# Optimization experiments

Hardware: AMD Instinct MI355X
Metric: run time of the kernel (lower is better)

Reference implementation:

```python
import jax, jax.numpy as jnp
import numpy as np

H = 64  # rnn_hidden_size


def _rnn_seq(x, W_ih, W_hh, b_ih, b_hh):
    """One tanh RNN layer over [B,T,D] -> full output sequence [B,T,H]."""
    pre = jnp.einsum('btd,hd->bth', x, W_ih) + b_ih  # input projection hoisted out of the scan
    h0 = jnp.zeros((x.shape[0], W_hh.shape[0]), x.dtype)
    def step(h, p_t):
        h = jnp.tanh(p_t + h @ W_hh.T + b_hh)
        return h, h
    _, ys = jax.lax.scan(step, h0, jnp.swapaxes(pre, 0, 1))  # scan over time
    return jnp.swapaxes(ys, 0, 1)


def _rnn_last(x, W_ih, W_hh, b_ih, b_hh):
    """One tanh RNN layer, returning only the last hidden state [B,H]."""
    pre = jnp.einsum('btd,hd->bth', x, W_ih) + b_ih
    h0 = jnp.zeros((x.shape[0], W_hh.shape[0]), x.dtype)
    def step(h, p_t):
        return jnp.tanh(p_t + h @ W_hh.T + b_hh), None
    h, _ = jax.lax.scan(step, h0, jnp.swapaxes(pre, 0, 1))
    return h


def setup_inputs() -> dict:
    key = jax.random.key(0)
    ks = jax.random.split(key, 32)
    B, T, D = 128, 4096, 3
    kr = 1.0 / np.sqrt(H)          # PyTorch RNN init bound
    u = lambda kk, shape, b: jax.random.uniform(kk, shape, jnp.float32, -b, b)
    inp = {
        'x': jax.random.normal(ks[0], (B, T, D), jnp.float32),
        'y': jax.random.normal(ks[1], (B, T, D), jnp.float32),
        'z': jax.random.normal(ks[2], (5,), jnp.float32),
        # rnn_empty, layer 0 (in=3) and layer 1 (in=64)
        'e_Wih0': u(ks[3], (H, D), kr), 'e_Whh0': u(ks[4], (H, H), kr),
        'e_bih0': u(ks[5], (H,), kr),  'e_bhh0': u(ks[6], (H,), kr),
        'e_Wih1': u(ks[7], (H, H), kr), 'e_Whh1': u(ks[8], (H, H), kr),
        'e_bih1': u(ks[9], (H,), kr),  'e_bhh1': u(ks[10], (H,), kr),
        # rnn_occupied
        'o_Wih0': u(ks[11], (H, D), kr), 'o_Whh0': u(ks[12], (H, H), kr),
        'o_bih0': u(ks[13], (H,), kr),  'o_bhh0': u(ks[14], (H,), kr),
        'o_Wih1': u(ks[15], (H, H), kr), 'o_Whh1': u(ks[16], (H, H), kr),
        'o_bih1': u(ks[17], (H,), kr),  'o_bhh1': u(ks[18], (H,), kr),
        # heads: fce/fco (64->2), fc1 (9->64), fc2 (64->5)
        'fce_w': u(ks[19], (2, H), kr), 'fce_b': u(ks[20], (2,), kr),
        'fco_w': u(ks[21], (2, H), kr), 'fco_b': u(ks[22], (2,), kr),
        'fc1_w': u(ks[23], (64, 9), 1.0 / np.sqrt(9)), 'fc1_b': u(ks[24], (64,), 1.0 / np.sqrt(9)),
        'fc2_w': u(ks[25], (5, 64), kr), 'fc2_b': u(ks[26], (5,), kr),
    }
    return inp


def reference(x, y, z,
              e_Wih0, e_Whh0, e_bih0, e_bhh0, e_Wih1, e_Whh1, e_bih1, e_bhh1,
              o_Wih0, o_Whh0, o_bih0, o_bhh0, o_Wih1, o_Whh1, o_bih1, o_bhh1,
              fce_w, fce_b, fco_w, fco_b, fc1_w, fc1_b, fc2_w, fc2_b):
    # two 2-layer tanh RNNs; last-timestep output of layer 2 == final hidden of layer 2
    hx = _rnn_last(_rnn_seq(x, e_Wih0, e_Whh0, e_bih0, e_bhh0),
                   e_Wih1, e_Whh1, e_bih1, e_bhh1)            # [B,H]
    hy = _rnn_last(_rnn_seq(y, o_Wih0, o_Whh0, o_bih0, o_bhh0),
                   o_Wih1, o_Whh1, o_bih1, o_bhh1)            # [B,H]
    e = hx @ fce_w.T + fce_b                                  # [B,2]
    o = hy @ fco_w.T + fco_b                                  # [B,2]
    zz = jnp.concatenate([e[0], o[0], z])                     # [9]
    h = jax.nn.relu(zz @ fc1_w.T + fc1_b)                     # [64]
    return h @ fc2_w.T + fc2_b                                # [5]
```

## Files before the change

kernel.cpp:

```cpp
#include <hip/hip_runtime.h>

#define T 4096
#define EP 8
#define RING 32
#define NEP (T / EP + 2)

typedef float f32x2 __attribute__((ext_vector_type(2)));
typedef unsigned long long u64;

__device__ __forceinline__ float fast_tanh(float x) {
    float e = __expf(2.0f * x);
    float r = __builtin_amdgcn_rcpf(e + 1.0f);
    return fmaf(-2.0f, r, 1.0f);
}

__device__ __forceinline__ float lane_bcast(float v, int j) {
    return __uint_as_float(__builtin_amdgcn_readlane(__float_as_uint(v), j));
}
__device__ __forceinline__ unsigned lane_bcast_u(float v, int j) {
    return (unsigned)__builtin_amdgcn_readlane(__float_as_uint(v), j);
}

#define PKFMA(acc, w, h) \
    asm("v_pk_fma_f32 %0, %1, %2, %0" : "+v"(acc) : "v"(w), "s"(h))

#define ANCHORP32(a) asm volatile("" : \
    "+v"((a)[0]),  "+v"((a)[1]),  "+v"((a)[2]),  "+v"((a)[3]),  \
    "+v"((a)[4]),  "+v"((a)[5]),  "+v"((a)[6]),  "+v"((a)[7]),  \
    "+v"((a)[8]),  "+v"((a)[9]),  "+v"((a)[10]), "+v"((a)[11]), \
    "+v"((a)[12]), "+v"((a)[13]), "+v"((a)[14]), "+v"((a)[15]), \
    "+v"((a)[16]), "+v"((a)[17]), "+v"((a)[18]), "+v"((a)[19]), \
    "+v"((a)[20]), "+v"((a)[21]), "+v"((a)[22]), "+v"((a)[23]), \
    "+v"((a)[24]), "+v"((a)[25]), "+v"((a)[26]), "+v"((a)[27]), \
    "+v"((a)[28]), "+v"((a)[29]), "+v"((a)[30]), "+v"((a)[31]))

#define ANCHOR16(a, b) asm volatile("" : \
    "+v"((a)[(b)+0]),  "+v"((a)[(b)+1]),  "+v"((a)[(b)+2]),  "+v"((a)[(b)+3]),  \
    "+v"((a)[(b)+4]),  "+v"((a)[(b)+5]),  "+v"((a)[(b)+6]),  "+v"((a)[(b)+7]),  \
    "+v"((a)[(b)+8]),  "+v"((a)[(b)+9]),  "+v"((a)[(b)+10]), "+v"((a)[(b)+11]), \
    "+v"((a)[(b)+12]), "+v"((a)[(b)+13]), "+v"((a)[(b)+14]), "+v"((a)[(b)+15]))
#define ANCHOR64(a) do { ANCHOR16(a, 0); ANCHOR16(a, 16); \
                         ANCHOR16(a, 32); ANCHOR16(a, 48); } while (0)

__device__ __forceinline__ u64 hpair(float hp, int j) {
    unsigned lo = lane_bcast_u(hp, j);
    unsigned hi = lane_bcast_u(hp, j + 1);
    return (u64)lo | ((u64)hi << 32);
}

__global__ void prep_kernel(const float* __restrict__ x, const float* __restrict__ y,
                            const float* __restrict__ eW, const float* __restrict__ ebi,
                            const float* __restrict__ ebh,
                            const float* __restrict__ oW, const float* __restrict__ obi,
                            const float* __restrict__ obh,
                            float* __restrict__ pre)
{
    int idx = blockIdx.x * blockDim.x + threadIdx.x;
    int i = idx & 63;
    int t = (idx >> 6) & (T - 1);
    int s = idx >> 18;
    const float* in = s ? y : x;
    const float* W  = s ? oW : eW;
    const float* bi = s ? obi : ebi;
    const float* bh = s ? obh : ebh;
    float v = bi[i] + bh[i]
            + W[i*3+0]*in[t*3+0] + W[i*3+1]*in[t*3+1] + W[i*3+2]*in[t*3+2];
    pre[idx] = v;
}

__global__ __launch_bounds__(256, 1) void seq_kernel(
    const float* __restrict__ pre,
    const float* __restrict__ eWhh0, const float* __restrict__ eWih1,
    const float* __restrict__ eWhh1, const float* __restrict__ ebih1,
    const float* __restrict__ ebhh1,
    const float* __restrict__ oWhh0, const float* __restrict__ oWih1,
    const float* __restrict__ oWhh1, const float* __restrict__ obih1,
    const float* __restrict__ obhh1,
    float* __restrict__ hlast)
{
    const int s    = blockIdx.x;
    const int wv   = threadIdx.x >> 6;
    const int lane = threadIdx.x & 63;

    __shared__ __align__(16) float h0ring[RING][64];
    __shared__ __align__(16) float qring[RING][64];

    const float* p = pre + s * T * 64;

    if (wv == 0) {
        const float* Whh0 = s ? oWhh0 : eWhh0;
        f32x2 w0p[32];
#pragma unroll
        for (int jp = 0; jp < 32; ++jp)
            w0p[jp] = ((const f32x2*)(Whh0 + lane * 64))[jp];

        float hp = 0.f;
        float pc[EP], pn[EP];
#pragma unroll
        for (int i = 0; i < EP; ++i) pc[i] = p[i * 64 + lane];

        for (int k = 0; k < NEP; ++k) {
            ANCHORP32(w0p);
            const int base = k * EP;
#pragma unroll
            for (int i = 0; i < EP; ++i) {
                int t = base + EP + i;
                pn[i] = (t < T) ? p[t * 64 + lane] : 0.f;
            }
            if (base < T) {
#pragma unroll
                for (int i = 0; i < EP; ++i) {
                    f32x2 acc0 = { pc[i], 0.f };
                    f32x2 acc1 = { 0.f, 0.f };
#pragma unroll
                    for (int jb = 0; jb < 64; jb += 8) {
                        u64 h01 = hpair(hp, jb + 0);
                        u64 h23 = hpair(hp, jb + 2);
                        u64 h45 = hpair(hp, jb + 4);
                        u64 h67 = hpair(hp, jb + 6);
                        PKFMA(acc0, w0p[(jb >> 1) + 0], h01);
                        PKFMA(acc1, w0p[(jb >> 1) + 1], h23);
                        PKFMA(acc0, w0p[(jb >> 1) + 2], h45);
                        PKFMA(acc1, w0p[(jb >> 1) + 3], h67);
                    }
                    hp = fast_tanh((acc0.x + acc0.y) + (acc1.x + acc1.y));
                    h0ring[(base + i) & (RING - 1)][lane] = hp;
                }
            }
#pragma unroll
            for (int i = 0; i < EP; ++i) pc[i] = pn[i];
            __syncthreads();
        }
    } else if (wv <= 2) {
        const float* Wih1 = s ? oWih1 : eWih1;
        const float  b1   = s ? (obih1[lane] + obhh1[lane])
                              : (ebih1[lane] + ebhh1[lane]);
        float wi[64];
#pragma unroll
        for (int j = 0; j < 64; ++j) wi[j] = Wih1[lane * 64 + j];

        const int i0 = (wv - 1) * (EP / 2);

        for (int k = 0; k < NEP; ++k) {
            ANCHOR64(wi);
            const int base = k * EP - EP;
            if (base >= 0 && base < T) {
#pragma unroll
                for (int i = 0; i < EP / 2; ++i) {
                    const int t = base + i0 + i;
                    const float4* hv = (const float4*)h0ring[t & (RING - 1)];
                    float q[4] = { b1, 0.f, 0.f, 0.f };
#pragma unroll
                    for (int j4 = 0; j4 < 16; ++j4) {
                        float4 u = hv[j4];
                        q[0] = fmaf(wi[4*j4+0], u.x, q[0]);
                        q[1] = fmaf(wi[4*j4+1], u.y, q[1]);
                        q[2] = fmaf(wi[4*j4+2], u.z, q[2]);
                        q[3] = fmaf(wi[4*j4+3], u.w, q[3]);
                    }
                    qring[t & (RING - 1)][lane] = (q[0] + q[1]) + (q[2] + q[3]);
                }
            }
            __syncthreads();
        }
    } else {
        const float* Whh1 = s ? oWhh1 : eWhh1;
        f32x2 w1p[32];
#pragma unroll
        for (int jp = 0; jp < 32; ++jp)
            w1p[jp] = ((const f32x2*)(Whh1 + lane * 64))[jp];

        float hp = 0.f;
        for (int k = 0; k < NEP; ++k) {
            ANCHORP32(w1p);
            const int base = k * EP - 2 * EP;
            if (base >= 0) {
                float qb[EP];
#pragma unroll
                for (int i = 0; i < EP; ++i)
                    qb[i] = qring[(base + i) & (RING - 1)][lane];
#pragma unroll
                for (int i = 0; i < EP; ++i) {
                    f32x2 acc0 = { qb[i], 0.f };
                    f32x2 acc1 = { 0.f, 0.f };
#pragma unroll
                    for (int jb = 0; jb < 64; jb += 8) {
                        u64 h01 = hpair(hp, jb + 0);
                        u64 h23 = hpair(hp, jb + 2);
                        u64 h45 = hpair(hp, jb + 4);
                        u64 h67 = hpair(hp, jb + 6);
                        PKFMA(acc0, w1p[(jb >> 1) + 0], h01);
                        PKFMA(acc1, w1p[(jb >> 1) + 1], h23);
                        PKFMA(acc0, w1p[(jb >> 1) + 2], h45);
                        PKFMA(acc1, w1p[(jb >> 1) + 3], h67);
                    }
                    hp = fast_tanh((acc0.x + acc0.y) + (acc1.x + acc1.y));
                }
            }
            __syncthreads();
        }
        hlast[s * 64 + lane] = hp;
    }
}

__global__ void head_kernel(const float* __restrict__ hlast,
                            const float* __restrict__ z,
                            const float* __restrict__ fce_w, const float* __restrict__ fce_b,
                            const float* __restrict__ fco_w, const float* __restrict__ fco_b,
                            const float* __restrict__ fc1_w, const float* __restrict__ fc1_b,
                            const float* __restrict__ fc2_w, const float* __restrict__ fc2_b,
                            float* __restrict__ out)
{
    const int lane = threadIdx.x;
    __shared__ float zz[9];
    __shared__ float hh[64];

    if (lane < 2) {
        float sacc = fce_b[lane];
        for (int j = 0; j < 64; ++j) sacc += fce_w[lane * 64 + j] * hlast[j];
        zz[lane] = sacc;
    } else if (lane < 4) {
        int r = lane - 2;
        float sacc = fco_b[r];
        for (int j = 0; j < 64; ++j) sacc += fco_w[r * 64 + j] * hlast[64 + j];
        zz[lane] = sacc;
    } else if (lane < 9) {
        zz[lane] = z[lane - 4];
    }
    __syncthreads();

    float sacc = fc1_b[lane];
#pragma unroll
    for (int j = 0; j < 9; ++j) sacc += fc1_w[lane * 9 + j] * zz[j];
    hh[lane] = fmaxf(sacc, 0.f);
    __syncthreads();

    if (lane < 5) {
        float o = fc2_b[lane];
        for (int i = 0; i < 64; ++i) o += fc2_w[lane * 64 + i] * hh[i];
        out[lane] = o;
    }
}

extern "C" void kernel_launch(void* const* d_in, const int* in_sizes, int n_in,
                              void* d_out, int out_size, void* d_ws, size_t ws_size,
                              hipStream_t stream)
{
    const float* x      = (const float*)d_in[0];
    const float* y      = (const float*)d_in[1];
    const float* z      = (const float*)d_in[2];
    const float* e_Wih0 = (const float*)d_in[3];
    const float* e_Whh0 = (const float*)d_in[4];
    const float* e_bih0 = (const float*)d_in[5];
    const float* e_bhh0 = (const float*)d_in[6];
    const float* e_Wih1 = (const float*)d_in[7];
    const float* e_Whh1 = (const float*)d_in[8];
    const float* e_bih1 = (const float*)d_in[9];
    const float* e_bhh1 = (const float*)d_in[10];
    const float* o_Wih0 = (const float*)d_in[11];
    const float* o_Whh0 = (const float*)d_in[12];
    const float* o_bih0 = (const float*)d_in[13];
    const float* o_bhh0 = (const float*)d_in[14];
    const float* o_Wih1 = (const float*)d_in[15];
    const float* o_Whh1 = (const float*)d_in[16];
    const float* o_bih1 = (const float*)d_in[17];
    const float* o_bhh1 = (const float*)d_in[18];
    const float* fce_w  = (const float*)d_in[19];
    const float* fce_b  = (const float*)d_in[20];
    const float* fco_w  = (const float*)d_in[21];
    const float* fco_b  = (const float*)d_in[22];
    const float* fc1_w  = (const float*)d_in[23];
    const float* fc1_b  = (const float*)d_in[24];
    const float* fc2_w  = (const float*)d_in[25];
    const float* fc2_b  = (const float*)d_in[26];

    float* pre   = (float*)d_ws;
    float* hlast = pre + 2 * T * 64;
    float* out   = (float*)d_out;

    prep_kernel<<<(2 * T * 64) / 256, 256, 0, stream>>>(
        x, y, e_Wih0, e_bih0, e_bhh0, o_Wih0, o_bih0, o_bhh0, pre);

    seq_kernel<<<2, 256, 0, stream>>>(
        pre,
        e_Whh0, e_Wih1, e_Whh1, e_bih1, e_bhh1,
        o_Whh0, o_Wih1, o_Whh1, o_bih1, o_bhh1,
        hlast);

    head_kernel<<<1, 64, 0, stream>>>(
        hlast, z, fce_w, fce_b, fco_w, fco_b, fc1_w, fc1_b, fc2_w, fc2_b, out);
}
```

Before: 1.096 ms.

## Interleave both RNN chains in one block to hide recurrence latency

Merges the two independent RNN stacks, previously one per block, into a single block. Each recurrent wave now advances both the x and y chains in lockstep, interleaving their readlane and packed-FMA instructions so one chain's latency can overlap the other's dependent work. The two projection waves now each handle one chain instead of splitting timesteps. This doubles per-wave register pressure for weights (128 VGPRs of packed weights) and doubles the instruction count per step on the critical serial wave, in exchange for filling dependency stalls and using one CU instead of two.

```diff
diff --git a/kernel.cpp b/kernel.cpp
--- a/kernel.cpp
+++ b/kernel.cpp
@@ -14,9 +14,6 @@
     return fmaf(-2.0f, r, 1.0f);
 }
 
-__device__ __forceinline__ float lane_bcast(float v, int j) {
-    return __uint_as_float(__builtin_amdgcn_readlane(__float_as_uint(v), j));
-}
 __device__ __forceinline__ unsigned lane_bcast_u(float v, int j) {
     return (unsigned)__builtin_amdgcn_readlane(__float_as_uint(v), j);
 }
@@ -78,77 +75,92 @@
     const float* __restrict__ obhh1,
     float* __restrict__ hlast)
 {
-    const int s    = blockIdx.x;
     const int wv   = threadIdx.x >> 6;
     const int lane = threadIdx.x & 63;
 
-    __shared__ __align__(16) float h0ring[RING][64];
-    __shared__ __align__(16) float qring[RING][64];
-
-    const float* p = pre + s * T * 64;
+    __shared__ __align__(16) float h0ring[2][RING][64];
+    __shared__ __align__(16) float qring[2][RING][64];
+
+    const float* pA = pre;
+    const float* pB = pre + T * 64;
 
     if (wv == 0) {
-        const float* Whh0 = s ? oWhh0 : eWhh0;
-        f32x2 w0p[32];
-#pragma unroll
-        for (int jp = 0; jp < 32; ++jp)
-            w0p[jp] = ((const f32x2*)(Whh0 + lane * 64))[jp];
-
-        float hp = 0.f;
-        float pc[EP], pn[EP];
-#pragma unroll
-        for (int i = 0; i < EP; ++i) pc[i] = p[i * 64 + lane];
+        f32x2 wAp[32], wBp[32];
+#pragma unroll
+        for (int jp = 0; jp < 32; ++jp) {
+            wAp[jp] = ((const f32x2*)(eWhh0 + lane * 64))[jp];
+            wBp[jp] = ((const f32x2*)(oWhh0 + lane * 64))[jp];
+        }
+
+        float hpA = 0.f, hpB = 0.f;
+        float pcA[EP], pcB[EP], pnA[EP], pnB[EP];
+#pragma unroll
+        for (int i = 0; i < EP; ++i) {
+            pcA[i] = pA[i * 64 + lane];
+            pcB[i] = pB[i * 64 + lane];
+        }
 
         for (int k = 0; k < NEP; ++k) {
-            ANCHORP32(w0p);
+            ANCHORP32(wAp);
+            ANCHORP32(wBp);
             const int base = k * EP;
 #pragma unroll
             for (int i = 0; i < EP; ++i) {
                 int t = base + EP + i;
-                pn[i] = (t < T) ? p[t * 64 + lane] : 0.f;
+                pnA[i] = (t < T) ? pA[t * 64 + lane] : 0.f;
+                pnB[i] = (t < T) ? pB[t * 64 + lane] : 0.f;
             }
             if (base < T) {
 #pragma unroll
                 for (int i = 0; i < EP; ++i) {
-                    f32x2 acc0 = { pc[i], 0.f };
-                    f32x2 acc1 = { 0.f, 0.f };
+                    f32x2 a0 = { pcA[i], 0.f }, a1 = { 0.f, 0.f };
+                    f32x2 b0 = { pcB[i], 0.f }, b1 = { 0.f, 0.f };
 #pragma unroll
                     for (int jb = 0; jb < 64; jb += 8) {
-                        u64 h01 = hpair(hp, jb + 0);
-                        u64 h23 = hpair(hp, jb + 2);
-                        u64 h45 = hpair(hp, jb + 4);
-                        u64 h67 = hpair(hp, jb + 6);
-                        PKFMA(acc0, w0p[(jb >> 1) + 0], h01);
-                        PKFMA(acc1, w0p[(jb >> 1) + 1], h23);
-                        PKFMA(acc0, w0p[(jb >> 1) + 2], h45);
-                        PKFMA(acc1, w0p[(jb >> 1) + 3], h67);
+                        u64 hA01 = hpair(hpA, jb + 0);
+                        u64 hB01 = hpair(hpB, jb + 0);
+                        u64 hA23 = hpair(hpA, jb + 2);
+                        u64 hB23 = hpair(hpB, jb + 2);
+                        u64 hA45 = hpair(hpA, jb + 4);
+                        u64 hB45 = hpair(hpB, jb + 4);
+                        u64 hA67 = hpair(hpA, jb + 6);
+                        u64 hB67 = hpair(hpB, jb + 6);
+                        PKFMA(a0, wAp[(jb >> 1) + 0], hA01);
+                        PKFMA(b0, wBp[(jb >> 1) + 0], hB01);
+                        PKFMA(a1, wAp[(jb >> 1) + 1], hA23);
+                        PKFMA(b1, wBp[(jb >> 1) + 1], hB23);
+                        PKFMA(a0, wAp[(jb >> 1) + 2], hA45);
+                        PKFMA(b0, wBp[(jb >> 1) + 2], hB45);
+                        PKFMA(a1, wAp[(jb >> 1) + 3], hA67);
+                        PKFMA(b1, wBp[(jb >> 1) + 3], hB67);
                     }
-                    hp = fast_tanh((acc0.x + acc0.y) + (acc1.x + acc1.y));
-                    h0ring[(base + i) & (RING - 1)][lane] = hp;
+                    hpA = fast_tanh((a0.x + a0.y) + (a1.x + a1.y));
+                    hpB = fast_tanh((b0.x + b0.y) + (b1.x + b1.y));
+                    h0ring[0][(base + i) & (RING - 1)][lane] = hpA;
+                    h0ring[1][(base + i) & (RING - 1)][lane] = hpB;
                 }
             }
 #pragma unroll
-            for (int i = 0; i < EP; ++i) pc[i] = pn[i];
+            for (int i = 0; i < EP; ++i) { pcA[i] = pnA[i]; pcB[i] = pnB[i]; }
             __syncthreads();
         }
     } else if (wv <= 2) {
-        const float* Wih1 = s ? oWih1 : eWih1;
-        const float  b1   = s ? (obih1[lane] + obhh1[lane])
-                              : (ebih1[lane] + ebhh1[lane]);
+        const int sidx = wv - 1;
+        const float* Wih1 = sidx ? oWih1 : eWih1;
+        const float  b1   = sidx ? (obih1[lane] + obhh1[lane])
+                                 : (ebih1[lane] + ebhh1[lane]);
         float wi[64];
 #pragma unroll
         for (int j = 0; j < 64; ++j) wi[j] = Wih1[lane * 64 + j];
-
-        const int i0 = (wv - 1) * (EP / 2);
 
         for (int k = 0; k < NEP; ++k) {
             ANCHOR64(wi);
             const int base = k * EP - EP;
             if (base >= 0 && base < T) {
 #pragma unroll
-                for (int i = 0; i < EP / 2; ++i) {
-                    const int t = base + i0 + i;
-                    const float4* hv = (const float4*)h0ring[t & (RING - 1)];
+                for (int i = 0; i < EP; ++i) {
+                    const int t = base + i;
+                    const float4* hv = (const float4*)h0ring[sidx][t & (RING - 1)];
                     float q[4] = { b1, 0.f, 0.f, 0.f };
 #pragma unroll
                     for (int j4 = 0; j4 < 16; ++j4) {
@@ -158,48 +170,62 @@
                         q[2] = fmaf(wi[4*j4+2], u.z, q[2]);
                         q[3] = fmaf(wi[4*j4+3], u.w, q[3]);
                     }
-                    qring[t & (RING - 1)][lane] = (q[0] + q[1]) + (q[2] + q[3]);
+                    qring[sidx][t & (RING - 1)][lane] = (q[0] + q[1]) + (q[2] + q[3]);
                 }
             }
             __syncthreads();
         }
     } else {
-        const float* Whh1 = s ? oWhh1 : eWhh1;
-        f32x2 w1p[32];
-#pragma unroll
-        for (int jp = 0; jp < 32; ++jp)
-            w1p[jp] = ((const f32x2*)(Whh1 + lane * 64))[jp];
-
-        float hp = 0.f;
+        f32x2 wAp[32], wBp[32];
+#pragma unroll
+        for (int jp = 0; jp < 32; ++jp) {
+            wAp[jp] = ((const f32x2*)(eWhh1 + lane * 64))[jp];
+            wBp[jp] = ((const f32x2*)(oWhh1 + lane * 64))[jp];
+        }
+
+        float hpA = 0.f, hpB = 0.f;
         for (int k = 0; k < NEP; ++k) {
-            ANCHORP32(w1p);
+            ANCHORP32(wAp);
+            ANCHORP32(wBp);
             const int base = k * EP - 2 * EP;
             if (base >= 0) {
-                float qb[EP];
-#pragma unroll
-                for (int i = 0; i < EP; ++i)
-                    qb[i] = qring[(base + i) & (RING - 1)][lane];
+                float qbA[EP], qbB[EP];
 #pragma unroll
                 for (int i = 0; i < EP; ++i) {
-                    f32x2 acc0 = { qb[i], 0.f };
-                    f32x2 acc1 = { 0.f, 0.f };
+                    qbA[i] = qring[0][(base + i) & (RING - 1)][lane];
+                    qbB[i] = qring[1][(base + i) & (RING - 1)][lane];
+                }
+#pragma unroll
+                for (int i = 0; i < EP; ++i) {
+                    f32x2 a0 = { qbA[i], 0.f }, a1 = { 0.f, 0.f };
+                    f32x2 b0 = { qbB[i], 0.f }, b1 = { 0.f, 0.f };
 #pragma unroll
                     for (int jb = 0; jb < 64; jb += 8) {
-                        u64 h01 = hpair(hp, jb + 0);
-                        u64 h23 = hpair(hp, jb + 2);
-                        u64 h45 = hpair(hp, jb + 4);
-                        u64 h67 = hpair(hp, jb + 6);
-                        PKFMA(acc0, w1p[(jb >> 1) + 0], h01);
-                        PKFMA(acc1, w1p[(jb >> 1) + 1], h23);
-                        PKFMA(acc0, w1p[(jb >> 1) + 2], h45);
-                        PKFMA(acc1, w1p[(jb >> 1) + 3], h67);
+                        u64 hA01 = hpair(hpA, jb + 0);
+                        u64 hB01 = hpair(hpB, jb + 0);
+                        u64 hA23 = hpair(hpA, jb + 2);
+                        u64 hB23 = hpair(hpB, jb + 2);
+                        u64 hA45 = hpair(hpA, jb + 4);
+                        u64 hB45 = hpair(hpB, jb + 4);
+                        u64 hA67 = hpair(hpA, jb + 6);
+                        u64 hB67 = hpair(hpB, jb + 6);
+                        PKFMA(a0, wAp[(jb >> 1) + 0], hA01);
+                        PKFMA(b0, wBp[(jb >> 1) + 0], hB01);
+                        PKFMA(a1, wAp[(jb >> 1) + 1], hA23);
+                        PKFMA(b1, wBp[(jb >> 1) + 1], hB23);
+                        PKFMA(a0, wAp[(jb >> 1) + 2], hA45);
+                        PKFMA(b0, wBp[(jb >> 1) + 2], hB45);
+                        PKFMA(a1, wAp[(jb >> 1) + 3], hA67);
+                        PKFMA(b1, wBp[(jb >> 1) + 3], hB67);
                     }
-                    hp = fast_tanh((acc0.x + acc0.y) + (acc1.x + acc1.y));
+                    hpA = fast_tanh((a0.x + a0.y) + (a1.x + a1.y));
+                    hpB = fast_tanh((b0.x + b0.y) + (b1.x + b1.y));
                 }
             }
             __syncthreads();
         }
-        hlast[s * 64 + lane] = hp;
+        hlast[lane]      = hpA;
+        hlast[64 + lane] = hpB;
     }
 }
 
@@ -281,7 +307,7 @@
     prep_kernel<<<(2 * T * 64) / 256, 256, 0, stream>>>(
         x, y, e_Wih0, e_bih0, e_bhh0, o_Wih0, o_bih0, o_bhh0, pre);
 
-    seq_kernel<<<2, 256, 0, stream>>>(
+    seq_kernel<<<1, 256, 0, stream>>>(
         pre,
         e_Whh0, e_Wih1, e_Whh1, e_bih1, e_bhh1,
         o_Whh0, o_Wih1, o_Whh1, o_bih1, o_bhh1,
```

New measurement: 1.986 ms. 81.2% more time.
